# Kernel optimization log

Hardware: AMD Instinct MI355X
Metric: run time of the kernel (lower is better)

## Reference

```python
import jax, jax.numpy as jnp
import numpy as np

V, E, H = 100000, 300, 256          # pretrained vectors, emb_dim, rep_dim
B, QLEN, DOC, S = 32, 32, 2048, 64  # batch, max_query_len, max_doc_len, max_num_sent
L = DOC // S                        # sentence length (lengths sum exactly to DOC)
VOCAB = V + 2                       # + extra token + padding idx


def _uniform(k, shape, scale):
    return jax.random.uniform(k, shape, jnp.float32, -scale, scale)


def setup_inputs() -> dict:
    key = jax.random.key(0)
    ks = jax.random.split(key, 16)
    s = 1.0 / np.sqrt(H)  # PyTorch GRU default init scale
    return {
        "queries": jax.random.randint(ks[0], (B, QLEN), 0, V),
        "query_lengths": jax.random.randint(ks[1], (B,), QLEN // 2, QLEN + 1).astype(jnp.int32),
        "docs": jax.random.randint(ks[2], (B, DOC), 0, V),
        "sentence_lengths": jnp.full((B, S), L, dtype=jnp.int32),
        "emb": jax.random.normal(ks[3], (VOCAB, E), jnp.float32) * 0.1,
        "q_wih": _uniform(ks[4], (3 * H, E), s), "q_whh": _uniform(ks[5], (3 * H, H), s),
        "q_bih": _uniform(ks[6], (3 * H,), s), "q_bhh": _uniform(ks[7], (3 * H,), s),
        "f_wih": _uniform(ks[8], (3 * H, E), s), "f_whh": _uniform(ks[9], (3 * H, H), s),
        "f_bih": _uniform(ks[10], (3 * H,), s), "f_bhh": _uniform(ks[11], (3 * H,), s),
        "b_wih": _uniform(ks[12], (3 * H, E), s), "b_whh": _uniform(ks[13], (3 * H, H), s),
        "b_bih": _uniform(ks[14], (3 * H,), s), "b_bhh": _uniform(ks[15], (3 * H,), s),
    }


def _gru(x, wih, whh, bih, bhh, reverse=False):
    # x: (B, T, E) -> hidden states (B, T, H); PyTorch GRU cell equations.
    xg = jnp.einsum('bte,ge->btg', x, wih) + bih  # (B, T, 3H) input projections

    def step(h, xt):
        gh = h @ whh.T + bhh
        ir, iz, inn = jnp.split(xt, 3, axis=-1)
        hr, hz, hn = jnp.split(gh, 3, axis=-1)
        r = jax.nn.sigmoid(ir + hr)
        z = jax.nn.sigmoid(iz + hz)
        n = jnp.tanh(inn + r * hn)
        hnew = (1.0 - z) * n + z * h
        return hnew, hnew

    h0 = jnp.zeros((x.shape[0], whh.shape[1]), x.dtype)
    _, hs = jax.lax.scan(step, h0, jnp.swapaxes(xg, 0, 1), reverse=reverse)
    return jnp.swapaxes(hs, 0, 1)


def reference(queries, query_lengths, docs, sentence_lengths, emb,
              q_wih, q_whh, q_bih, q_bhh,
              f_wih, f_whh, f_bih, f_bhh,
              b_wih, b_whh, b_bih, b_bhh):
    q_emb = emb[queries]  # (B, QLEN, E)
    d_emb = emb[docs]     # (B, DOC, E)

    # Ragged per-sentence mean pooling (_get_facts) as one segment-mean per doc.
    def seg_mean(xb, lens):
        ids = jnp.repeat(jnp.arange(S), lens, total_repeat_length=DOC)
        sums = jax.ops.segment_sum(xb, ids, num_segments=S)
        return sums / jnp.maximum(lens, 1)[:, None].astype(xb.dtype)

    facts = jax.vmap(seg_mean)(d_emb, sentence_lengths)  # (B, S, E)

    # Question GRU: hidden state at the last valid token (pack_padded semantics).
    q_hs = _gru(q_emb, q_wih, q_whh, q_bih, q_bhh)
    q_rep = q_hs[jnp.arange(B), query_lengths - 1][:, None, :]  # (B, 1, H)

    # Input fusion: bidirectional GRU over facts, fwd + bwd halves summed (dropout off / eval).
    f_out = (_gru(facts, f_wih, f_whh, f_bih, f_bhh)
             + _gru(facts, b_wih, b_whh, b_bih, b_bhh, reverse=True))  # (B, S, H)

    num_facts = jnp.sum(sentence_lengths > 0, axis=1)
    return q_rep, f_out, num_facts
```

## Files before the change

kernel.cpp:

```cpp
#include <hip/hip_runtime.h>

#define Bn   32
#define QL   32
#define DOCn 2048
#define Sn   64
#define En   300
#define Hn   256

typedef short bf16x8 __attribute__((ext_vector_type(8)));
typedef short s16x4  __attribute__((ext_vector_type(4)));
typedef float f32x4  __attribute__((ext_vector_type(4)));

static __device__ __forceinline__ float b2f(short s){
  unsigned int u = ((unsigned int)(unsigned short)s) << 16;
  float f; __builtin_memcpy(&f, &u, 4); return f;
}
static __device__ __forceinline__ short f2b(float f){
  unsigned int u; __builtin_memcpy(&u, &f, 4);
  u = u + 0x7fffu + ((u >> 16) & 1u);
  return (short)(u >> 16);
}
static __device__ __forceinline__ float sigm(float x){ return 1.0f/(1.0f+__expf(-x)); }
static __device__ __forceinline__ float tanhx(float x){ return 1.0f - 2.0f/(__expf(2.0f*x)+1.0f); }
static __device__ __forceinline__ f32x4 mfma16(bf16x8 a, bf16x8 b, f32x4 c){
  return __builtin_amdgcn_mfma_f32_16x16x32_bf16(a, b, c, 0, 0, 0);
}
static __device__ __forceinline__ void bar_lgkm(){
  asm volatile("s_waitcnt lgkmcnt(0)\n\ts_barrier" ::: "memory");
}

__global__ __launch_bounds__(256) void k_facts(
    const int* __restrict__ docs, const int* __restrict__ slens,
    const float* __restrict__ emb, short* __restrict__ facts,
    float* __restrict__ dout)
{
  __shared__ int pref[2*Sn];
  const int blk = blockIdx.x;
  const int b = blk >> 6, s = blk & 63;
  const int tid = threadIdx.x;
  if (tid < Sn){
    const int v = slens[b*Sn + tid];
    int x = v;
#pragma unroll
    for (int d = 1; d < 64; d <<= 1){
      const int y = __shfl_up(x, d, 64);
      if (tid >= d) x += y;
    }
    pref[tid] = x - v;
    pref[Sn + tid] = v;
    if (s == 0){
      const unsigned long long m = __ballot(v > 0);
      if (tid == 0) dout[Bn*Hn + (long)Bn*Sn*Hn + b] = (float)__popcll(m);
    }
  }
  __syncthreads();
  const int off = pref[s];
  const int len = pref[Sn + s];
  const int e0 = tid;
  float a0 = 0.f, a1 = 0.f;
  const int* dtok = docs + b*DOCn + off;
  int tk = (len > 0) ? dtok[0] : 0;
  for (int l = 0; l < len; ++l){
    const int tkn = (l + 1 < len) ? dtok[l+1] : 0;
    const float* row = emb + (long)tk*En;
    a0 += row[e0];
    if (e0 + 256 < En) a1 += row[e0+256];
    tk = tkn;
  }
  const float inv = 1.0f / (float)(len > 0 ? len : 1);
  short* frow = facts + ((long)b*Sn + s)*En;
  frow[e0] = f2b(a0*inv);
  if (e0 + 256 < En) frow[e0+256] = f2b(a1*inv);
}

__global__ __launch_bounds__(256) void k_xg(
    const short* __restrict__ facts,
    const int* __restrict__ queries, const float* __restrict__ emb,
    const float* __restrict__ q_wih, const float* __restrict__ q_bih,
    const float* __restrict__ q_bhh,
    const float* __restrict__ f_wih, const float* __restrict__ f_bih,
    const float* __restrict__ f_bhh,
    const float* __restrict__ b_wih, const float* __restrict__ b_bih,
    const float* __restrict__ b_bhh,
    short* __restrict__ q_xgi, short* __restrict__ f_xgi,
    short* __restrict__ b_xgi)
{
  const int z = blockIdx.z;
  const int bm = blockIdx.x, bn = blockIdx.y;
  if (z == 2 && bm >= 16) return;

  const float* wih = (z == 0) ? f_wih : (z == 1) ? b_wih : q_wih;
  const float* bih = (z == 0) ? f_bih : (z == 1) ? b_bih : q_bih;
  const float* bhh = (z == 0) ? f_bhh : (z == 1) ? b_bhh : q_bhh;
  short*       xgi = (z == 0) ? f_xgi : (z == 1) ? b_xgi : q_xgi;
  const bool isq = (z == 2);

  __shared__ alignas(16) short Al[2][64][40];
  const int tid = threadIdx.x;
  const int l = tid & 63, w = tid >> 6;
  const int wm = w & 1, wn = w >> 1;
  const int l15 = l & 15, lq = l >> 4;

  bf16x8 bfr[2][10];
#pragma unroll
  for (int nt = 0; nt < 2; ++nt){
    const int g = bn*64 + wn*32 + nt*16 + l15;
    const float* wr = wih + (long)g*En;
#pragma unroll
    for (int kk = 0; kk < 10; ++kk){
      const int k0 = kk*32 + lq*8;
      bf16x8 v;
      if (k0 + 7 < En){
        const f32x4 f0 = *(const f32x4*)(wr + k0);
        const f32x4 f1 = *(const f32x4*)(wr + k0 + 4);
#pragma unroll
        for (int j = 0; j < 4; ++j){ v[j] = f2b(f0[j]); v[4+j] = f2b(f1[j]); }
      } else {
#pragma unroll
        for (int j = 0; j < 8; ++j){ const int k = k0 + j; v[j] = (k < En) ? f2b(wr[k]) : (short)0; }
      }
      bfr[nt][kk] = v;
    }
  }

  const int arow = l;
  const int ak8  = w*8;
  const float* asrc_q = nullptr;
  const short* asrc_f = nullptr;
  if (isq){
    const int tok = queries[bm*64 + arow];
    asrc_q = emb + (long)tok*En;
  } else {
    asrc_f = facts + (long)(bm*64 + arow)*En;
  }

  s16x4 a0_, a1_;
#define LDA_(KK) do{ const int k0_ = (KK)*32 + ak8; \
    if (isq){ \
      if (k0_ + 7 < En){ const f32x4 f0_ = *(const f32x4*)(asrc_q+k0_), f1_ = *(const f32x4*)(asrc_q+k0_+4); \
        a0_ = (s16x4){f2b(f0_[0]),f2b(f0_[1]),f2b(f0_[2]),f2b(f0_[3])}; \
        a1_ = (s16x4){f2b(f1_[0]),f2b(f1_[1]),f2b(f1_[2]),f2b(f1_[3])}; } \
      else { _Pragma("unroll") for (int j=0;j<4;++j){ const int ka_=k0_+j, kb_=k0_+4+j; \
        a0_[j] = (ka_<En)? f2b(asrc_q[ka_]) : (short)0; a1_[j] = (kb_<En)? f2b(asrc_q[kb_]) : (short)0; } } \
    } else { \
      if (k0_ + 7 < En){ a0_ = *(const s16x4*)(asrc_f+k0_); a1_ = *(const s16x4*)(asrc_f+k0_+4); } \
      else { _Pragma("unroll") for (int j=0;j<4;++j){ const int ka_=k0_+j, kb_=k0_+4+j; \
        a0_[j] = (ka_<En)? asrc_f[ka_] : (short)0; a1_[j] = (kb_<En)? asrc_f[kb_] : (short)0; } } \
    } }while(0)
#define STA_(BUF) do{ *(s16x4*)&Al[BUF][arow][ak8] = a0_; *(s16x4*)&Al[BUF][arow][ak8+4] = a1_; }while(0)

  LDA_(0); STA_(0);
  __syncthreads();

  f32x4 acc[2][2] = {};
#pragma unroll
  for (int kk = 0; kk < 10; ++kk){
    if (kk < 9) LDA_(kk+1);
#pragma unroll
    for (int mt = 0; mt < 2; ++mt){
      bf16x8 a = *(const bf16x8*)&Al[kk&1][wm*32 + mt*16 + l15][lq*8];
      acc[mt][0] = mfma16(a, bfr[0][kk], acc[mt][0]);
      acc[mt][1] = mfma16(a, bfr[1][kk], acc[mt][1]);
    }
    if (kk < 9) STA_((kk+1)&1);
    __syncthreads();
  }
#undef LDA_
#undef STA_

#pragma unroll
  for (int nt = 0; nt < 2; ++nt){
    const int cg = bn*64 + wn*32 + nt*16 + l15;
    float bias = bih[cg];
    if (cg < 512) bias += bhh[cg];
    const int gate = cg >> 8, hc = cg & 255;
#pragma unroll
    for (int mt = 0; mt < 2; ++mt){
      const int r0 = bm*64 + wm*32 + mt*16 + lq*4;
#pragma unroll
      for (int p = 0; p < 4; ++p){
        const int r = r0 + p;
        const int row = isq ? ((r & 31)*32 + (r >> 5)) : ((r & 63)*32 + (r >> 6));
        xgi[(long)row*1024 + hc*4 + gate] = f2b(acc[mt][nt][p] + bias);
      }
    }
  }
}

__global__ __launch_bounds__(1024) void k_gru(
    const short* __restrict__ q_xg, const short* __restrict__ f_xg,
    const short* __restrict__ b_xg,
    const float* __restrict__ q_whh, const float* __restrict__ q_bhh,
    const float* __restrict__ f_whh, const float* __restrict__ f_bhh,
    const float* __restrict__ b_whh, const float* __restrict__ b_bhh,
    const int* __restrict__ qlens,
    float* __restrict__ dout)
{
  __shared__ alignas(16) short hl[2*16*264];
  __shared__ alignas(16) short wl[7*1024*8];

  const int gru = blockIdx.x >> 1;
  const int mh  = blockIdx.x & 1;
  const int tid = threadIdx.x;
  const int l = tid & 63, w = tid >> 6;
  const int l15 = l & 15, lq = l >> 4;

  const float* whh = (gru == 0) ? q_whh : (gru == 1) ? f_whh : b_whh;
  const float* bhh = (gru == 0) ? q_bhh : (gru == 1) ? f_bhh : b_bhh;
  const short* xgp = (gru == 0) ? q_xg  : (gru == 1) ? f_xg  : b_xg;
  const int T = (gru == 0) ? QL : Sn;

  const int c = w*16 + l15;

  bf16x8 wf[3][6];
  float bhn = 0.f;
#pragma unroll
  for (int gi = 0; gi < 3; ++gi){
    const int g = gi*256 + c;
    const float* wr = whh + (long)g*Hn;
#pragma unroll
    for (int kk = 0; kk < 8; ++kk){
      const f32x4 f0 = *(const f32x4*)(wr + kk*32 + lq*8);
      const f32x4 f1 = *(const f32x4*)(wr + kk*32 + lq*8 + 4);
      bf16x8 v;
#pragma unroll
      for (int j = 0; j < 4; ++j){ v[j] = f2b(f0[j]); v[4+j] = f2b(f1[j]); }
      if (kk < 5 || (kk == 5 && gi < 2)) wf[gi][kk] = v;
      else if (kk == 5)                  *(bf16x8*)&wl[(6*1024 + tid)*8] = v;
      else                               *(bf16x8*)&wl[(((kk-6)*3 + gi)*1024 + tid)*8] = v;
    }
    if (gi == 2) bhn = bhh[g];
  }

  float hreg[4] = {};
  int qlen_m[4];
#pragma unroll
  for (int p = 0; p < 4; ++p) qlen_m[p] = (gru == 0) ? qlens[mh*16 + lq*4 + p] : -1;

  const int vo = (mh*16 + lq*4)*1024 + c*4;
  float* qdst  = dout + (mh*16 + lq*4)*Hn + c;
  float* fbase = dout + Bn*Hn + (long)(mh*16 + lq*4)*(Sn*Hn) + c;

  s16x4 preA[4], preB[4];

#define TOF(TT) ((gru == 2) ? (T - 1 - (TT)) : (TT))
#define LOADP(PRE, TI) do{ const short* sb_ = xgp + (long)(TI)*32768 + vo; \
    PRE[0] = *(const s16x4*)(sb_); \
    PRE[1] = *(const s16x4*)(sb_ + 1024); \
    PRE[2] = *(const s16x4*)(sb_ + 2048); \
    PRE[3] = *(const s16x4*)(sb_ + 3072); }while(0)

#define GRU_STEP(TT, DOM, HIN, HOUT, PRE) do{ \
    f32x4 acc0 = (f32x4){0.f,0.f,0.f,0.f}; \
    f32x4 acc1 = (f32x4){0.f,0.f,0.f,0.f}; \
    f32x4 acc2 = (f32x4){bhn,bhn,bhn,bhn}; \
    if (DOM){ \
      _Pragma("unroll") for (int kk = 0; kk < 5; ++kk){ \
        const bf16x8 a = *(const bf16x8*)&(HIN)[l15*264 + kk*32 + lq*8]; \
        acc0 = mfma16(a, wf[0][kk], acc0); \
        acc1 = mfma16(a, wf[1][kk], acc1); \
        acc2 = mfma16(a, wf[2][kk], acc2); \
      } \
      { const bf16x8 a = *(const bf16x8*)&(HIN)[l15*264 + 5*32 + lq*8]; \
        const bf16x8 w2 = *(const bf16x8*)&wl[(6*1024 + tid)*8]; \
        acc0 = mfma16(a, wf[0][5], acc0); \
        acc1 = mfma16(a, wf[1][5], acc1); \
        acc2 = mfma16(a, w2, acc2); } \
      { const bf16x8 a = *(const bf16x8*)&(HIN)[l15*264 + 6*32 + lq*8]; \
        const bf16x8 w0 = *(const bf16x8*)&wl[(0*1024 + tid)*8]; \
        const bf16x8 w1 = *(const bf16x8*)&wl[(1*1024 + tid)*8]; \
        const bf16x8 w2 = *(const bf16x8*)&wl[(2*1024 + tid)*8]; \
        acc0 = mfma16(a, w0, acc0); \
        acc1 = mfma16(a, w1, acc1); \
        acc2 = mfma16(a, w2, acc2); } \
      { const bf16x8 a = *(const bf16x8*)&(HIN)[l15*264 + 7*32 + lq*8]; \
        const bf16x8 w0 = *(const bf16x8*)&wl[(3*1024 + tid)*8]; \
        const bf16x8 w1 = *(const bf16x8*)&wl[(4*1024 + tid)*8]; \
        const bf16x8 w2 = *(const bf16x8*)&wl[(5*1024 + tid)*8]; \
        acc0 = mfma16(a, w0, acc0); \
        acc1 = mfma16(a, w1, acc1); \
        acc2 = mfma16(a, w2, acc2); } \
    } \
    const int t_ = TOF(TT); \
    _Pragma("unroll") for (int p = 0; p < 4; ++p){ \
      const float ir = b2f(PRE[p][0]), iz = b2f(PRE[p][1]), in_ = b2f(PRE[p][2]); \
      const float rr = sigm(ir + acc0[p]); \
      const float zz = sigm(iz + acc1[p]); \
      const float nn = tanhx(in_ + rr*acc2[p]); \
      const float hn = (1.0f - zz)*nn + zz*hreg[p]; \
      hreg[p] = hn; \
      (HOUT)[(lq*4 + p)*264 + c] = f2b(hn); \
      if (gru == 0){ if (t_ == qlen_m[p] - 1) qdst[p*Hn] = hn; } \
      else { atomicAdd(fbase + p*(Sn*Hn) + t_*Hn, hn); } \
    } \
  }while(0)

  short* h0 = hl;
  short* h1 = hl + 4224;

  LOADP(preA, TOF(0));
  LOADP(preB, TOF(1));
  __builtin_amdgcn_sched_barrier(0);
  GRU_STEP(0, 0, h1, h0, preA);
  bar_lgkm();
  LOADP(preA, TOF(2));
  __builtin_amdgcn_sched_barrier(0);
  GRU_STEP(1, 1, h0, h1, preB);
  bar_lgkm();

  for (int tt = 2; tt < T; tt += 2){
    const int tiB = (tt+1 < T) ? (tt+1) : (T-1);
    LOADP(preB, TOF(tiB));
    __builtin_amdgcn_sched_barrier(0);
    GRU_STEP(tt, 1, h1, h0, preA);
    bar_lgkm();
    const int tiA = (tt+2 < T) ? (tt+2) : (T-1);
    LOADP(preA, TOF(tiA));
    __builtin_amdgcn_sched_barrier(0);
    GRU_STEP(tt+1, 1, h0, h1, preB);
    bar_lgkm();
  }
#undef TOF
#undef LOADP
#undef GRU_STEP
}

extern "C" void kernel_launch(void* const* d_in, const int* in_sizes, int n_in,
                              void* d_out, int out_size, void* d_ws, size_t ws_size,
                              hipStream_t stream)
{
  const int*   queries = (const int*)d_in[0];
  const int*   qlens   = (const int*)d_in[1];
  const int*   docs    = (const int*)d_in[2];
  const int*   slens   = (const int*)d_in[3];
  const float* emb     = (const float*)d_in[4];
  const float* q_wih   = (const float*)d_in[5];
  const float* q_whh   = (const float*)d_in[6];
  const float* q_bih   = (const float*)d_in[7];
  const float* q_bhh   = (const float*)d_in[8];
  const float* f_wih   = (const float*)d_in[9];
  const float* f_whh   = (const float*)d_in[10];
  const float* f_bih   = (const float*)d_in[11];
  const float* f_bhh   = (const float*)d_in[12];
  const float* b_wih   = (const float*)d_in[13];
  const float* b_whh   = (const float*)d_in[14];
  const float* b_bih   = (const float*)d_in[15];
  const float* b_bhh   = (const float*)d_in[16];

  char* wsb = (char*)d_ws;
  short* f_xgi = (short*)(wsb);
  short* b_xgi = (short*)(wsb +  4194304);
  short* q_xgi = (short*)(wsb +  8388608);
  short* facts = (short*)(wsb + 10485760);

  float* dout = (float*)d_out;

  k_facts<<<dim3(Bn*Sn), 256, 0, stream>>>(docs, slens, emb, facts, dout);
  k_xg   <<<dim3(32, 12, 3), 256, 0, stream>>>(facts, queries, emb,
                                               q_wih, q_bih, q_bhh,
                                               f_wih, f_bih, f_bhh,
                                               b_wih, b_bih, b_bhh,
                                               q_xgi, f_xgi, b_xgi);
  k_gru  <<<dim3(6), 1024, 0, stream>>>(q_xgi, f_xgi, b_xgi, q_whh, q_bhh,
                                        f_whh, f_bhh, b_whh, b_bhh,
                                        qlens, dout);
}
```

Before: 524.6 us.

## Pre-convert input weights to padded bf16 and double the xg M-tile

Extra blocks in the facts kernel now convert all three input-projection weight matrices to bf16 once, padded to 320 columns. The projection GEMM then loads its B fragments directly as bf16 vectors instead of converting fp32 per block. Facts rows are padded to 320 and zero-filled, which removes the tail-bound branches. Each xg block now computes 128 rows instead of 64, halving the block count and the redundant weight loads, at the cost of more registers, more LDS and fewer blocks to spread across CUs.

Measured after the change: 518.7 us. Within noise of the previous version (-1.1%).

```diff
diff --git a/kernel.cpp b/kernel.cpp
--- a/kernel.cpp
+++ b/kernel.cpp
@@ -31,13 +31,31 @@
 
 __global__ __launch_bounds__(256) void k_facts(
     const int* __restrict__ docs, const int* __restrict__ slens,
-    const float* __restrict__ emb, short* __restrict__ facts,
+    const float* __restrict__ emb,
+    const float* __restrict__ f_wih, const float* __restrict__ b_wih,
+    const float* __restrict__ q_wih,
+    short* __restrict__ facts, short* __restrict__ wcvt,
     float* __restrict__ dout)
 {
+  const int tid = threadIdx.x;
+
+  if (blockIdx.x >= 2048){
+    const int rg0 = (blockIdx.x - 2048)*8;
+#pragma unroll
+    for (int rr = 0; rr < 8; ++rr){
+      const int rg = rg0 + rr;
+      const int z = rg / 768, g = rg % 768;
+      const float* src = ((z == 0) ? f_wih : (z == 1) ? b_wih : q_wih) + (long)g*En;
+      short* dst = wcvt + (long)rg*320;
+      for (int c = tid; c < 320; c += 256)
+        dst[c] = (c < En) ? f2b(src[c]) : (short)0;
+    }
+    return;
+  }
+
   __shared__ int pref[2*Sn];
   const int blk = blockIdx.x;
   const int b = blk >> 6, s = blk & 63;
-  const int tid = threadIdx.x;
   if (tid < Sn){
     const int v = slens[b*Sn + tid];
     int x = v;
@@ -68,97 +86,85 @@
     tk = tkn;
   }
   const float inv = 1.0f / (float)(len > 0 ? len : 1);
-  short* frow = facts + ((long)b*Sn + s)*En;
+  short* frow = facts + ((long)b*Sn + s)*320;
   frow[e0] = f2b(a0*inv);
-  if (e0 + 256 < En) frow[e0+256] = f2b(a1*inv);
+  if (e0 < 64) frow[e0+256] = (e0 + 256 < En) ? f2b(a1*inv) : (short)0;
 }
 
 __global__ __launch_bounds__(256) void k_xg(
-    const short* __restrict__ facts,
+    const short* __restrict__ facts, const short* __restrict__ wcvt,
     const int* __restrict__ queries, const float* __restrict__ emb,
-    const float* __restrict__ q_wih, const float* __restrict__ q_bih,
-    const float* __restrict__ q_bhh,
-    const float* __restrict__ f_wih, const float* __restrict__ f_bih,
-    const float* __restrict__ f_bhh,
-    const float* __restrict__ b_wih, const float* __restrict__ b_bih,
-    const float* __restrict__ b_bhh,
+    const float* __restrict__ q_bih, const float* __restrict__ q_bhh,
+    const float* __restrict__ f_bih, const float* __restrict__ f_bhh,
+    const float* __restrict__ b_bih, const float* __restrict__ b_bhh,
     short* __restrict__ q_xgi, short* __restrict__ f_xgi,
     short* __restrict__ b_xgi)
 {
   const int z = blockIdx.z;
   const int bm = blockIdx.x, bn = blockIdx.y;
-  if (z == 2 && bm >= 16) return;
-
-  const float* wih = (z == 0) ? f_wih : (z == 1) ? b_wih : q_wih;
+  const bool isq = (z == 2);
+  if (isq && bm >= 8) return;
+
   const float* bih = (z == 0) ? f_bih : (z == 1) ? b_bih : q_bih;
   const float* bhh = (z == 0) ? f_bhh : (z == 1) ? b_bhh : q_bhh;
   short*       xgi = (z == 0) ? f_xgi : (z == 1) ? b_xgi : q_xgi;
-  const bool isq = (z == 2);
-
-  __shared__ alignas(16) short Al[2][64][40];
+
+  __shared__ alignas(16) short Al[2][128][40];
   const int tid = threadIdx.x;
   const int l = tid & 63, w = tid >> 6;
   const int wm = w & 1, wn = w >> 1;
   const int l15 = l & 15, lq = l >> 4;
+  const int ak8 = w*8;
 
   bf16x8 bfr[2][10];
 #pragma unroll
   for (int nt = 0; nt < 2; ++nt){
     const int g = bn*64 + wn*32 + nt*16 + l15;
-    const float* wr = wih + (long)g*En;
-#pragma unroll
-    for (int kk = 0; kk < 10; ++kk){
-      const int k0 = kk*32 + lq*8;
-      bf16x8 v;
-      if (k0 + 7 < En){
-        const f32x4 f0 = *(const f32x4*)(wr + k0);
-        const f32x4 f1 = *(const f32x4*)(wr + k0 + 4);
-#pragma unroll
-        for (int j = 0; j < 4; ++j){ v[j] = f2b(f0[j]); v[4+j] = f2b(f1[j]); }
-      } else {
-#pragma unroll
-        for (int j = 0; j < 8; ++j){ const int k = k0 + j; v[j] = (k < En) ? f2b(wr[k]) : (short)0; }
-      }
-      bfr[nt][kk] = v;
-    }
-  }
-
-  const int arow = l;
-  const int ak8  = w*8;
-  const float* asrc_q = nullptr;
-  const short* asrc_f = nullptr;
+    const short* wr = wcvt + ((long)z*768 + g)*320;
+#pragma unroll
+    for (int kk = 0; kk < 10; ++kk)
+      bfr[nt][kk] = *(const bf16x8*)&wr[kk*32 + lq*8];
+  }
+
+  const short* asrc_f0 = nullptr; const short* asrc_f1 = nullptr;
+  const float* asrc_q0 = nullptr; const float* asrc_q1 = nullptr;
   if (isq){
-    const int tok = queries[bm*64 + arow];
-    asrc_q = emb + (long)tok*En;
+    asrc_q0 = emb + (long)queries[bm*128 + l]*En;
+    asrc_q1 = emb + (long)queries[bm*128 + 64 + l]*En;
   } else {
-    asrc_f = facts + (long)(bm*64 + arow)*En;
-  }
-
-  s16x4 a0_, a1_;
+    asrc_f0 = facts + (long)(bm*128 + l)*320;
+    asrc_f1 = facts + (long)(bm*128 + 64 + l)*320;
+  }
+
+  bf16x8 va0, va1;
 #define LDA_(KK) do{ const int k0_ = (KK)*32 + ak8; \
-    if (isq){ \
-      if (k0_ + 7 < En){ const f32x4 f0_ = *(const f32x4*)(asrc_q+k0_), f1_ = *(const f32x4*)(asrc_q+k0_+4); \
-        a0_ = (s16x4){f2b(f0_[0]),f2b(f0_[1]),f2b(f0_[2]),f2b(f0_[3])}; \
-        a1_ = (s16x4){f2b(f1_[0]),f2b(f1_[1]),f2b(f1_[2]),f2b(f1_[3])}; } \
-      else { _Pragma("unroll") for (int j=0;j<4;++j){ const int ka_=k0_+j, kb_=k0_+4+j; \
-        a0_[j] = (ka_<En)? f2b(asrc_q[ka_]) : (short)0; a1_[j] = (kb_<En)? f2b(asrc_q[kb_]) : (short)0; } } \
+    if (!isq){ \
+      va0 = *(const bf16x8*)(asrc_f0 + k0_); \
+      va1 = *(const bf16x8*)(asrc_f1 + k0_); \
+    } else if (k0_ + 7 < En){ \
+      const f32x4 p0 = *(const f32x4*)(asrc_q0+k0_), p1 = *(const f32x4*)(asrc_q0+k0_+4); \
+      const f32x4 p2 = *(const f32x4*)(asrc_q1+k0_), p3 = *(const f32x4*)(asrc_q1+k0_+4); \
+      _Pragma("unroll") for (int j = 0; j < 4; ++j){ \
+        va0[j] = f2b(p0[j]); va0[4+j] = f2b(p1[j]); \
+        va1[j] = f2b(p2[j]); va1[4+j] = f2b(p3[j]); } \
     } else { \
-      if (k0_ + 7 < En){ a0_ = *(const s16x4*)(asrc_f+k0_); a1_ = *(const s16x4*)(asrc_f+k0_+4); } \
-      else { _Pragma("unroll") for (int j=0;j<4;++j){ const int ka_=k0_+j, kb_=k0_+4+j; \
-        a0_[j] = (ka_<En)? asrc_f[ka_] : (short)0; a1_[j] = (kb_<En)? asrc_f[kb_] : (short)0; } } \
+      _Pragma("unroll") for (int j = 0; j < 8; ++j){ const int k_ = k0_ + j; \
+        va0[j] = (k_ < En) ? f2b(asrc_q0[k_]) : (short)0; \
+        va1[j] = (k_ < En) ? f2b(asrc_q1[k_]) : (short)0; } \
     } }while(0)
-#define STA_(BUF) do{ *(s16x4*)&Al[BUF][arow][ak8] = a0_; *(s16x4*)&Al[BUF][arow][ak8+4] = a1_; }while(0)
+#define STA_(BUF) do{ *(bf16x8*)&Al[BUF][l][ak8] = va0; \
+    *(bf16x8*)&Al[BUF][64 + l][ak8] = va1; }while(0)
 
   LDA_(0); STA_(0);
   __syncthreads();
 
-  f32x4 acc[2][2] = {};
+  f32x4 acc[4][2] = {};
 #pragma unroll
   for (int kk = 0; kk < 10; ++kk){
     if (kk < 9) LDA_(kk+1);
 #pragma unroll
-    for (int mt = 0; mt < 2; ++mt){
-      bf16x8 a = *(const bf16x8*)&Al[kk&1][wm*32 + mt*16 + l15][lq*8];
+    for (int mt = 0; mt < 4; ++mt){
+      bf16x8 a = *(const bf16x8*)&Al[kk&1][wm*64 + mt*16 + l15][lq*8];
       acc[mt][0] = mfma16(a, bfr[0][kk], acc[mt][0]);
       acc[mt][1] = mfma16(a, bfr[1][kk], acc[mt][1]);
     }
@@ -175,8 +181,8 @@
     if (cg < 512) bias += bhh[cg];
     const int gate = cg >> 8, hc = cg & 255;
 #pragma unroll
-    for (int mt = 0; mt < 2; ++mt){
-      const int r0 = bm*64 + wm*32 + mt*16 + lq*4;
+    for (int mt = 0; mt < 4; ++mt){
+      const int r0 = bm*128 + wm*64 + mt*16 + lq*4;
 #pragma unroll
       for (int p = 0; p < 4; ++p){
         const int r = r0 + p;
@@ -352,14 +358,16 @@
   short* b_xgi = (short*)(wsb +  4194304);
   short* q_xgi = (short*)(wsb +  8388608);
   short* facts = (short*)(wsb + 10485760);
+  short* wcvt  = (short*)(wsb + 11796480);
 
   float* dout = (float*)d_out;
 
-  k_facts<<<dim3(Bn*Sn), 256, 0, stream>>>(docs, slens, emb, facts, dout);
-  k_xg   <<<dim3(32, 12, 3), 256, 0, stream>>>(facts, queries, emb,
-                                               q_wih, q_bih, q_bhh,
-                                               f_wih, f_bih, f_bhh,
-                                               b_wih, b_bih, b_bhh,
+  k_facts<<<dim3(2048 + 288), 256, 0, stream>>>(docs, slens, emb,
+                                                f_wih, b_wih, q_wih,
+                                                facts, wcvt, dout);
+  k_xg   <<<dim3(16, 12, 3), 256, 0, stream>>>(facts, wcvt, queries, emb,
+                                               q_bih, q_bhh, f_bih, f_bhh,
+                                               b_bih, b_bhh,
                                                q_xgi, f_xgi, b_xgi);
   k_gru  <<<dim3(6), 1024, 0, stream>>>(q_xgi, f_xgi, b_xgi, q_whh, q_bhh,
                                         f_whh, f_bhh, b_whh, b_bhh,
```
